# Performance work log

Measured on AMD Instinct MI355X. Metric: run time of the kernel, lower is better.

The kernel has to match this reference:

```python
import jax, jax.numpy as jnp
import numpy as np

# The torch code implements pixel shifts via bmm with sparse permutation
# matrices: T[i,i+1]=1. bmm(x, T) moves column j-1 -> j (shift right, zero col 0);
# bmm(x, T^T) shifts left; bmm(T, x) moves row j+1 -> j (shift up, zero last row);
# bmm(T^T, x) shifts down. We implement these directly as pad+slice gathers.

def _shift_right(x):  # [B,H,W]
    return jnp.pad(x[:, :, :-1], ((0, 0), (0, 0), (1, 0)))

def _shift_left(x):
    return jnp.pad(x[:, :, 1:], ((0, 0), (0, 0), (0, 1)))

def _shift_up(x):
    return jnp.pad(x[:, 1:, :], ((0, 0), (0, 1), (0, 0)))

def _shift_down(x):
    return jnp.pad(x[:, :-1, :], ((0, 0), (1, 0), (0, 0)))

def _bce_sum(p, t):
    # torch.nn.BCELoss(reduction='sum') clamps log terms at -100
    logp = jnp.clip(jnp.log(p), -100.0, None)
    log1mp = jnp.clip(jnp.log1p(-p), -100.0, None)
    return -jnp.sum(t * logp + (1.0 - t) * log1mp)

def setup_inputs() -> dict:
    key = jax.random.key(0)
    k1, k2, k3 = jax.random.split(key, 3)
    B, C, H, W = 16, 8, 512, 512
    c_map = jax.random.normal(k1, (B, C, H, W), dtype=jnp.float32)
    target = jax.random.bernoulli(k2, 0.5, (B, 1, H, W)).astype(jnp.float32)
    con_target = jax.random.bernoulli(k3, 0.5, (B, C, H, W)).astype(jnp.float32)
    return {"c_map": c_map, "target": target, "con_target": con_target}

def reference(c_map, target, con_target):
    p = jax.nn.sigmoid(c_map)  # [B,8,H,W]

    sum_conn = jnp.sum(con_target, axis=1)  # [B,H,W]
    edge = ((sum_conn < 8.0) & (sum_conn > 0.0)).astype(p.dtype)

    c0, c1, c2, c3 = p[:, 0], p[:, 1], p[:, 2], p[:, 3]
    c4, c5, c6, c7 = p[:, 4], p[:, 5], p[:, 6], p[:, 7]

    right = _shift_right(c4)
    left = _shift_left(c3)
    left_bottom = _shift_left(_shift_down(c5))
    right_above = _shift_right(_shift_up(c2))
    left_above = _shift_left(_shift_up(c0))
    bottom = _shift_down(c6)
    up = _shift_up(c1)
    right_bottom = _shift_right(_shift_down(c7))

    a1 = c3 * right
    a2 = c4 * left
    a3 = c1 * bottom
    a4 = c6 * up
    a5 = c2 * left_bottom
    a6 = c5 * right_above
    a7 = c0 * right_bottom
    a8 = c7 * left_above

    vote_out = jnp.stack([a7, a3, a5, a1, a2, a6, a4, a8], axis=1)  # [B,8,H,W]

    glo_map = jnp.mean(vote_out, axis=1)       # [B,H,W]
    pred_mask_min = jnp.min(vote_out, axis=1)  # [B,H,W]
    decouple_map = glo_map * (1.0 - edge) + (1.0 - pred_mask_min) * edge

    de_loss = _bce_sum(decouple_map[:, None], target)
    conmap_l = _bce_sum(p, con_target)
    bimap_l = _bce_sum(vote_out, con_target)
    return 0.8 * conmap_l + de_loss + 0.2 * bimap_l
```

## Files before the change

kernel.cpp:

```cpp
#include <hip/hip_runtime.h>
#include <math.h>

#define NB 16
#define NC 8
#define HH 512
#define WW 512
#define HW (HH * WW)
#define CHW (NC * HW)
#define NSEG 8

typedef const __attribute__((address_space(1))) void* gvp;
typedef __attribute__((address_space(3))) void*       lvp;

__device__ __forceinline__ float bce_term(float t, float p) {
    float q = (t > 0.5f) ? p : (1.0f - p);
    return -fmaxf(__logf(q), -100.0f);
}

__global__ __launch_bounds__(256) void bicon_loss_kernel(
    const float* __restrict__ c_map,
    const float* __restrict__ target,
    const float* __restrict__ con_target,
    float* __restrict__ out)
{
    __shared__ float buf[4][2][24][64];
    __shared__ float wsum[4];

    const int tid  = threadIdx.x;
    const int wave = tid >> 6;
    const int lane = tid & 63;
    const int wid  = blockIdx.x * 4 + wave;
    const int b    = wid >> 8;
    const int h0   = (wid & 255) << 1;

    const float* dma_ptr[6];
    #pragma unroll
    for (int s = 0; s < 6; ++s) {
        const int pp = s * 4 + (lane >> 4);
        const float* base;
        if (pp < 22) {
            int ch, rel;
            if (pp < 3)       { ch = 5 + pp;  rel = -1; }
            else if (pp < 11) { ch = pp - 3;  rel = 0;  }
            else if (pp < 19) { ch = pp - 11; rel = 1;  }
            else              { ch = pp - 19; rel = 2;  }
            int rr = h0 + rel; rr = rr < 0 ? 0 : (rr > HH - 1 ? HH - 1 : rr);
            base = c_map + b * CHW + ch * HW + rr * WW;
        } else {
            base = target + b * HW + (h0 + pp - 22) * WW;
        }
        dma_ptr[s] = base + (lane & 15) * 4;
    }

    {
    }
    const int k    = lane < 12 ? lane : 0;
    const int kk4  = (k >> 1) * 4;
    const int dirR = ((k & 1) == 0);
    const int ch_e = dirR ? ((0x253235 >> kk4) & 15) : ((0x074047 >> kk4) & 15);
    const int rel_e = ((0x312210 >> kk4) & 15) - 1;
    int rre = h0 + rel_e; rre = rre < 0 ? 0 : (rre > HH - 1 ? HH - 1 : rre);
    const float* eptr = c_map + b * CHW + ch_e * HW + rre * WW + (dirR ? 64 : -1);

    float (*mybuf)[24][64] = buf[wave];

    #pragma unroll
    for (int s = 0; s < 6; ++s)
        __builtin_amdgcn_global_load_lds((gvp)dma_ptr[s], (lvp)&mybuf[0][s * 4][0], 16, 0, 0);
    float ex_cur = eptr[0];

    const bool hu  = (h0 > 0);
    const bool hd2 = (h0 < HH - 2);

    float acc_con = 0.0f, acc_bi = 0.0f, acc_de = 0.0f;

    for (int t = 0; t < NSEG; ++t) {
        const int par = t & 1;
        if (t + 1 < NSEG) {
            const int w1 = (t + 1) << 6;
            #pragma unroll
            for (int s = 0; s < 6; ++s)
                __builtin_amdgcn_global_load_lds((gvp)(dma_ptr[s] + w1),
                                                 (lvp)&mybuf[(t + 1) & 1][s * 4][0], 16, 0, 0);
            __builtin_amdgcn_s_waitcnt(0x0F76);
        } else {
            __builtin_amdgcn_s_waitcnt(0x0F70);
        }
        asm volatile("" ::: "memory");

        const int w0 = t << 6;
        const int gw = w0 + lane;
        const bool wl = (gw > 0), wr = (gw < WW - 1);

        const float* ctb = con_target + b * CHW + h0 * WW + gw;
        float tv0[8], tv1[8];
        #pragma unroll
        for (int c = 0; c < 8; ++c) { tv0[c] = ctb[c * HW]; tv1[c] = ctb[c * HW + WW]; }
        float ex_next = 0.0f;
        if (t + 1 < NSEG) ex_next = eptr[(t + 1) << 6];

        float u[22], xc[16];
        #pragma unroll
        for (int pp = 0; pp < 22; ++pp) {
            const float x = mybuf[par][pp][lane];
            if (pp >= 3 && pp < 19) xc[pp - 3] = x;
            u[pp] = 1.0f + __expf(-x);
        }
        const float tg0 = mybuf[par][22][lane];
        const float tg1 = mybuf[par][23][lane];
        const float ue  = 1.0f + __expf(-ex_cur);

        #define U0(c) u[3 + (c)]
        #define U1(c) u[11 + (c)]
        auto SHP = [&](float v, int ek) -> float {
            float s = __shfl(v, (lane + 1) & 63, 64);
            float e = __shfl(ue, ek, 64);
            return (lane == 63) ? e : s;
        };
        auto SHM = [&](float v, int ek) -> float {
            float s = __shfl(v, (lane + 63) & 63, 64);
            float e = __shfl(ue, ek, 64);
            return (lane == 0) ? e : s;
        };
        auto VOTE = [&](float uc, float un, bool valid) -> float {
            return valid ? __fdividef(1.0f, uc * un) : 0.0f;
        };

        const float m4  = SHM(U0(4), 3);
        const float m3  = SHP(U0(3), 2);
        const float n5  = SHP(u[0], 0);
        const float n6  = u[1];
        const float n7  = SHM(u[2], 1);
        const float dn1 = U1(1);
        const float dn2 = SHP(U1(2), 4);
        const float dn0 = SHM(U1(0), 5);
        const float a1 = VOTE(U0(3), m4, wl);
        const float a2 = VOTE(U0(4), m3, wr);
        const float a3 = VOTE(U0(1), n6, hu);
        const float a4 = VOTE(U0(6), dn1, true);
        const float a5 = VOTE(U0(2), n5, hu && wr);
        const float a6 = VOTE(U0(5), dn2, wr);
        const float a7 = VOTE(U0(0), n7, hu && wl);
        const float a8 = VOTE(U0(7), dn0, wl);

        const float m4b  = SHM(U1(4), 7);
        const float m3b  = SHP(U1(3), 6);
        const float n5b  = SHP(U0(5), 8);
        const float n6b  = U0(6);
        const float n7b  = SHM(U0(7), 9);
        const float dn1b = u[20];
        const float dn2b = SHP(u[21], 10);
        const float dn0b = SHM(u[19], 11);
        const float b1 = VOTE(U1(3), m4b, wl);
        const float b2 = VOTE(U1(4), m3b, wr);
        const float b3 = VOTE(U1(1), n6b, true);
        const float b4 = VOTE(U1(6), dn1b, hd2);
        const float b5 = VOTE(U1(2), n5b, wr);
        const float b6 = VOTE(U1(5), dn2b, hd2 && wr);
        const float b7 = VOTE(U1(0), n7b, wl);
        const float b8 = VOTE(U1(7), dn0b, hd2 && wl);

        #pragma unroll
        for (int c = 0; c < 8; ++c) {
            acc_con += __logf(u[3 + c])  + (tv0[c] > 0.5f ? 0.0f : xc[c]);
            acc_con += __logf(u[11 + c]) + (tv1[c] > 0.5f ? 0.0f : xc[8 + c]);
        }

        const float v0[8] = { a7, a3, a5, a1, a2, a6, a4, a8 };
        const float v1[8] = { b7, b3, b5, b1, b2, b6, b4, b8 };
        float sc0 = 0.0f, sc1 = 0.0f;
        #pragma unroll
        for (int c = 0; c < 8; ++c) { sc0 += tv0[c]; sc1 += tv1[c]; }
        #pragma unroll
        for (int c = 0; c < 8; ++c) {
            acc_bi += bce_term(tv0[c], v0[c]);
            acc_bi += bce_term(tv1[c], v1[c]);
        }
        const float g0 = (a1 + a2 + a3 + a4 + a5 + a6 + a7 + a8) * 0.125f;
        const float g1 = (b1 + b2 + b3 + b4 + b5 + b6 + b7 + b8) * 0.125f;
        float mn0 = v0[0], mn1 = v1[0];
        #pragma unroll
        for (int c = 1; c < 8; ++c) { mn0 = fminf(mn0, v0[c]); mn1 = fminf(mn1, v1[c]); }
        const bool  e0 = (sc0 < 8.0f) && (sc0 > 0.0f);
        const bool  e1 = (sc1 < 8.0f) && (sc1 > 0.0f);
        const float d0 = e0 ? (1.0f - mn0) : g0;
        const float d1 = e1 ? (1.0f - mn1) : g1;
        acc_de += bce_term(tg0, d0);
        acc_de += bce_term(tg1, d1);

        ex_cur = ex_next;
        #undef U0
        #undef U1
    }

    float local = fmaf(0.8f, acc_con, fmaf(0.2f, acc_bi, acc_de));
    #pragma unroll
    for (int off = 32; off > 0; off >>= 1)
        local += __shfl_down(local, off, 64);
    if (lane == 0) wsum[wave] = local;
    __syncthreads();
    if (tid == 0) atomicAdd(out, wsum[0] + wsum[1] + wsum[2] + wsum[3]);
}

extern "C" void kernel_launch(void* const* d_in, const int* in_sizes, int n_in,
                              void* d_out, int out_size, void* d_ws, size_t ws_size,
                              hipStream_t stream) {
    const float* c_map      = (const float*)d_in[0];
    const float* target     = (const float*)d_in[1];
    const float* con_target = (const float*)d_in[2];
    float* out = (float*)d_out;

    hipMemsetAsync(out, 0, sizeof(float), stream);

    const int blocks = (NB * (HH / 2)) / 4;
    bicon_loss_kernel<<<blocks, 256, 0, stream>>>(c_map, target, con_target, out);
}
```

Measured before the change: 306.6 us.

## Stage con_target via LDS DMA and fold BCE logs into products

Result: no change. 308.7 us (+0.7%).

```diff
diff --git a/kernel.cpp b/kernel.cpp
--- a/kernel.cpp
+++ b/kernel.cpp
@@ -2,11 +2,10 @@
 #include <math.h>
 
 #define NB 16
-#define NC 8
 #define HH 512
 #define WW 512
 #define HW (HH * WW)
-#define CHW (NC * HW)
+#define CHW (8 * HW)
 #define NSEG 8
 
 typedef const __attribute__((address_space(1))) void* gvp;
@@ -17,25 +16,24 @@
     return -fmaxf(__logf(q), -100.0f);
 }
 
-__global__ __launch_bounds__(256) void bicon_loss_kernel(
+__global__ __launch_bounds__(128, 2) void bicon_loss_kernel(
     const float* __restrict__ c_map,
     const float* __restrict__ target,
     const float* __restrict__ con_target,
     float* __restrict__ out)
 {
-    __shared__ float buf[4][2][24][64];
-    __shared__ float wsum[4];
+    __shared__ float buf[2][2][40][64];
 
     const int tid  = threadIdx.x;
     const int wave = tid >> 6;
     const int lane = tid & 63;
-    const int wid  = blockIdx.x * 4 + wave;
+    const int wid  = blockIdx.x * 2 + wave;
     const int b    = wid >> 8;
     const int h0   = (wid & 255) << 1;
 
-    const float* dma_ptr[6];
+    const float* dma_ptr[10];
     #pragma unroll
-    for (int s = 0; s < 6; ++s) {
+    for (int s = 0; s < 10; ++s) {
         const int pp = s * 4 + (lane >> 4);
         const float* base;
         if (pp < 22) {
@@ -46,28 +44,31 @@
             else              { ch = pp - 19; rel = 2;  }
             int rr = h0 + rel; rr = rr < 0 ? 0 : (rr > HH - 1 ? HH - 1 : rr);
             base = c_map + b * CHW + ch * HW + rr * WW;
+        } else if (pp < 24) {
+            base = target + b * HW + (h0 + pp - 22) * WW;
+        } else if (pp < 32) {
+            base = con_target + b * CHW + (pp - 24) * HW + h0 * WW;
         } else {
-            base = target + b * HW + (h0 + pp - 22) * WW;
+            base = con_target + b * CHW + (pp - 32) * HW + (h0 + 1) * WW;
         }
         dma_ptr[s] = base + (lane & 15) * 4;
     }
 
-    {
-    }
-    const int k    = lane < 12 ? lane : 0;
-    const int kk4  = (k >> 1) * 4;
-    const int dirR = ((k & 1) == 0);
-    const int ch_e = dirR ? ((0x253235 >> kk4) & 15) : ((0x074047 >> kk4) & 15);
+    const int k     = lane < 12 ? lane : 0;
+    const int kk4   = (k >> 1) * 4;
+    const int dirR  = ((k & 1) == 0);
+    const int ch_e  = dirR ? ((0x253235 >> kk4) & 15) : ((0x074047 >> kk4) & 15);
     const int rel_e = ((0x312210 >> kk4) & 15) - 1;
     int rre = h0 + rel_e; rre = rre < 0 ? 0 : (rre > HH - 1 ? HH - 1 : rre);
     const float* eptr = c_map + b * CHW + ch_e * HW + rre * WW + (dirR ? 64 : -1);
 
-    float (*mybuf)[24][64] = buf[wave];
-
+    float (*mybuf)[40][64] = buf[wave];
+
+    float ex_cur = eptr[0];
+    asm volatile("" ::: "memory");
     #pragma unroll
-    for (int s = 0; s < 6; ++s)
+    for (int s = 0; s < 10; ++s)
         __builtin_amdgcn_global_load_lds((gvp)dma_ptr[s], (lvp)&mybuf[0][s * 4][0], 16, 0, 0);
-    float ex_cur = eptr[0];
 
     const bool hu  = (h0 > 0);
     const bool hd2 = (h0 < HH - 2);
@@ -76,39 +77,40 @@
 
     for (int t = 0; t < NSEG; ++t) {
         const int par = t & 1;
+        float ex_next = 0.0f;
         if (t + 1 < NSEG) {
             const int w1 = (t + 1) << 6;
+            ex_next = eptr[w1];
+            asm volatile("" ::: "memory");
             #pragma unroll
-            for (int s = 0; s < 6; ++s)
+            for (int s = 0; s < 10; ++s)
                 __builtin_amdgcn_global_load_lds((gvp)(dma_ptr[s] + w1),
                                                  (lvp)&mybuf[(t + 1) & 1][s * 4][0], 16, 0, 0);
-            __builtin_amdgcn_s_waitcnt(0x0F76);
+            __builtin_amdgcn_s_waitcnt(0x0F7B);
         } else {
             __builtin_amdgcn_s_waitcnt(0x0F70);
         }
         asm volatile("" ::: "memory");
 
-        const int w0 = t << 6;
-        const int gw = w0 + lane;
+        const int gw = (t << 6) + lane;
         const bool wl = (gw > 0), wr = (gw < WW - 1);
 
-        const float* ctb = con_target + b * CHW + h0 * WW + gw;
-        float tv0[8], tv1[8];
-        #pragma unroll
-        for (int c = 0; c < 8; ++c) { tv0[c] = ctb[c * HW]; tv1[c] = ctb[c * HW + WW]; }
-        float ex_next = 0.0f;
-        if (t + 1 < NSEG) ex_next = eptr[(t + 1) << 6];
-
-        float u[22], xc[16];
-        #pragma unroll
-        for (int pp = 0; pp < 22; ++pp) {
-            const float x = mybuf[par][pp][lane];
-            if (pp >= 3 && pp < 19) xc[pp - 3] = x;
-            u[pp] = 1.0f + __expf(-x);
-        }
+        float xv[22];
+        #pragma unroll
+        for (int pp = 0; pp < 22; ++pp) xv[pp] = mybuf[par][pp][lane];
         const float tg0 = mybuf[par][22][lane];
         const float tg1 = mybuf[par][23][lane];
-        const float ue  = 1.0f + __expf(-ex_cur);
+        float tv0[8], tv1[8];
+        #pragma unroll
+        for (int c = 0; c < 8; ++c) {
+            tv0[c] = mybuf[par][24 + c][lane];
+            tv1[c] = mybuf[par][32 + c][lane];
+        }
+
+        float u[22];
+        #pragma unroll
+        for (int pp = 0; pp < 22; ++pp) u[pp] = 1.0f + __expf(-xv[pp]);
+        const float ue = 1.0f + __expf(-ex_cur);
 
         #define U0(c) u[3 + (c)]
         #define U1(c) u[11 + (c)]
@@ -122,71 +124,67 @@
             float e = __shfl(ue, ek, 64);
             return (lane == 0) ? e : s;
         };
-        auto VOTE = [&](float uc, float un, bool valid) -> float {
-            return valid ? __fdividef(1.0f, uc * un) : 0.0f;
+
+        const float m4   = SHM(U0(4), 3),  m3   = SHP(U0(3), 2);
+        const float n5   = SHP(u[0], 0),   n6   = u[1],  n7 = SHM(u[2], 1);
+        const float dn1  = U1(1), dn2 = SHP(U1(2), 4), dn0 = SHM(U1(0), 5);
+        const float m4b  = SHM(U1(4), 7),  m3b  = SHP(U1(3), 6);
+        const float n5b  = SHP(U0(5), 8),  n6b  = U0(6), n7b = SHM(U0(7), 9);
+        const float dn1b = u[20], dn2b = SHP(u[21], 10), dn0b = SHM(u[19], 11);
+
+        float wv0[8], wv1[8];
+        bool  va0[8], va1[8];
+        wv0[0] = U0(0) * n7;   va0[0] = hu && wl;
+        wv0[1] = U0(1) * n6;   va0[1] = hu;
+        wv0[2] = U0(2) * n5;   va0[2] = hu && wr;
+        wv0[3] = U0(3) * m4;   va0[3] = wl;
+        wv0[4] = U0(4) * m3;   va0[4] = wr;
+        wv0[5] = U0(5) * dn2;  va0[5] = wr;
+        wv0[6] = U0(6) * dn1;  va0[6] = true;
+        wv0[7] = U0(7) * dn0;  va0[7] = wl;
+        wv1[0] = U1(0) * n7b;  va1[0] = wl;
+        wv1[1] = U1(1) * n6b;  va1[1] = true;
+        wv1[2] = U1(2) * n5b;  va1[2] = wr;
+        wv1[3] = U1(3) * m4b;  va1[3] = wl;
+        wv1[4] = U1(4) * m3b;  va1[4] = wr;
+        wv1[5] = U1(5) * dn2b; va1[5] = hd2 && wr;
+        wv1[6] = U1(6) * dn1b; va1[6] = hd2;
+        wv1[7] = U1(7) * dn0b; va1[7] = hd2 && wl;
+
+        float P0 = 1.0f, P1 = 1.0f, lin = 0.0f;
+        #pragma unroll
+        for (int c = 0; c < 8; ++c) {
+            P0 *= u[3 + c];   lin += (tv0[c] > 0.5f) ? 0.0f : xv[3 + c];
+            P1 *= u[11 + c];  lin += (tv1[c] > 0.5f) ? 0.0f : xv[11 + c];
+        }
+        acc_con += __logf(P0) + __logf(P1) + lin;
+
+        auto row_loss = [&](const float* wv, const bool* va, const float* tv,
+                            float tg) {
+            float pW0 = 1.0f, pW1 = 1.0f, pQ0 = 1.0f, pQ1 = 1.0f;
+            float corr = 0.0f, sumc = 0.0f, sumv = 0.0f, vmin = 1.0f;
+            #pragma unroll
+            for (int c = 0; c < 8; ++c) {
+                const float tt = tv[c];
+                const float w  = wv[c];
+                const bool  va_c = va[c];
+                sumc += tt;
+                const float wp = va_c ? w : 1.0f;
+                const float qq = (va_c && tt < 0.5f) ? (w - 1.0f) : 1.0f;
+                corr += (!va_c && tt > 0.5f) ? 100.0f : 0.0f;
+                if (c < 4) { pW0 *= wp; pQ0 *= qq; }
+                else       { pW1 *= wp; pQ1 *= qq; }
+                const float vv = va_c ? __fdividef(1.0f, w) : 0.0f;
+                sumv += vv;
+                vmin = fminf(vmin, vv);
+            }
+            acc_bi += __logf(pW0) + __logf(pW1) - __logf(pQ0) - __logf(pQ1) + corr;
+            const bool edge = (sumc < 8.0f) && (sumc > 0.0f);
+            const float dec = edge ? (1.0f - vmin) : (0.125f * sumv);
+            acc_de += bce_term(tg, dec);
         };
-
-        const float m4  = SHM(U0(4), 3);
-        const float m3  = SHP(U0(3), 2);
-        const float n5  = SHP(u[0], 0);
-        const float n6  = u[1];
-        const float n7  = SHM(u[2], 1);
-        const float dn1 = U1(1);
-        const float dn2 = SHP(U1(2), 4);
-        const float dn0 = SHM(U1(0), 5);
-        const float a1 = VOTE(U0(3), m4, wl);
-        const float a2 = VOTE(U0(4), m3, wr);
-        const float a3 = VOTE(U0(1), n6, hu);
-        const float a4 = VOTE(U0(6), dn1, true);
-        const float a5 = VOTE(U0(2), n5, hu && wr);
-        const float a6 = VOTE(U0(5), dn2, wr);
-        const float a7 = VOTE(U0(0), n7, hu && wl);
-        const float a8 = VOTE(U0(7), dn0, wl);
-
-        const float m4b  = SHM(U1(4), 7);
-        const float m3b  = SHP(U1(3), 6);
-        const float n5b  = SHP(U0(5), 8);
-        const float n6b  = U0(6);
-        const float n7b  = SHM(U0(7), 9);
-        const float dn1b = u[20];
-        const float dn2b = SHP(u[21], 10);
-        const float dn0b = SHM(u[19], 11);
-        const float b1 = VOTE(U1(3), m4b, wl);
-        const float b2 = VOTE(U1(4), m3b, wr);
-        const float b3 = VOTE(U1(1), n6b, true);
-        const float b4 = VOTE(U1(6), dn1b, hd2);
-        const float b5 = VOTE(U1(2), n5b, wr);
-        const float b6 = VOTE(U1(5), dn2b, hd2 && wr);
-        const float b7 = VOTE(U1(0), n7b, wl);
-        const float b8 = VOTE(U1(7), dn0b, hd2 && wl);
-
-        #pragma unroll
-        for (int c = 0; c < 8; ++c) {
-            acc_con += __logf(u[3 + c])  + (tv0[c] > 0.5f ? 0.0f : xc[c]);
-            acc_con += __logf(u[11 + c]) + (tv1[c] > 0.5f ? 0.0f : xc[8 + c]);
-        }
-
-        const float v0[8] = { a7, a3, a5, a1, a2, a6, a4, a8 };
-        const float v1[8] = { b7, b3, b5, b1, b2, b6, b4, b8 };
-        float sc0 = 0.0f, sc1 = 0.0f;
-        #pragma unroll
-        for (int c = 0; c < 8; ++c) { sc0 += tv0[c]; sc1 += tv1[c]; }
-        #pragma unroll
-        for (int c = 0; c < 8; ++c) {
-            acc_bi += bce_term(tv0[c], v0[c]);
-            acc_bi += bce_term(tv1[c], v1[c]);
-        }
-        const float g0 = (a1 + a2 + a3 + a4 + a5 + a6 + a7 + a8) * 0.125f;
-        const float g1 = (b1 + b2 + b3 + b4 + b5 + b6 + b7 + b8) * 0.125f;
-        float mn0 = v0[0], mn1 = v1[0];
-        #pragma unroll
-        for (int c = 1; c < 8; ++c) { mn0 = fminf(mn0, v0[c]); mn1 = fminf(mn1, v1[c]); }
-        const bool  e0 = (sc0 < 8.0f) && (sc0 > 0.0f);
-        const bool  e1 = (sc1 < 8.0f) && (sc1 > 0.0f);
-        const float d0 = e0 ? (1.0f - mn0) : g0;
-        const float d1 = e1 ? (1.0f - mn1) : g1;
-        acc_de += bce_term(tg0, d0);
-        acc_de += bce_term(tg1, d1);
+        row_loss(wv0, va0, tv0, tg0);
+        row_loss(wv1, va1, tv1, tg1);
 
         ex_cur = ex_next;
         #undef U0
@@ -197,9 +195,7 @@
     #pragma unroll
     for (int off = 32; off > 0; off >>= 1)
         local += __shfl_down(local, off, 64);
-    if (lane == 0) wsum[wave] = local;
-    __syncthreads();
-    if (tid == 0) atomicAdd(out, wsum[0] + wsum[1] + wsum[2] + wsum[3]);
+    if (lane == 0) atomicAdd(out, local);
 }
 
 extern "C" void kernel_launch(void* const* d_in, const int* in_sizes, int n_in,
@@ -212,6 +208,6 @@
 
     hipMemsetAsync(out, 0, sizeof(float), stream);
 
-    const int blocks = (NB * (HH / 2)) / 4;
-    bicon_loss_kernel<<<blocks, 256, 0, stream>>>(c_map, target, con_target, out);
+    const int blocks = (NB * (HH / 2)) / 2;
+    bicon_loss_kernel<<<blocks, 128, 0, stream>>>(c_map, target, con_target, out);
 }
```
